# Performance work log

Measured on AMD Instinct MI355X. Metric: run time of the kernel, lower is better.

The kernel has to match this reference:

```python
import jax, jax.numpy as jnp
import numpy as np

# Production-scale sparse-voxel constants (Waymo-ish stride-8 grid)
N = 1_000_000   # active voxels across the batch
C = 128         # NUM_BEV_FEATURES
B, Z, Y, X = 8, 4, 468, 468  # batch size and spatial_shape (z, y, x)


def setup_inputs() -> dict:
    key = jax.random.key(0)
    kf, kb, kz, ky, kx = jax.random.split(key, 5)
    features = jax.random.normal(kf, (N, C), dtype=jnp.float32)
    b = jax.random.randint(kb, (N,), 0, B, dtype=jnp.int32)
    z = jax.random.randint(kz, (N,), 0, Z, dtype=jnp.int32)
    y = jax.random.randint(ky, (N,), 0, Y, dtype=jnp.int32)
    x = jax.random.randint(kx, (N,), 0, X, dtype=jnp.int32)
    indices = jnp.stack([b, z, y, x], axis=1)  # [N, 4]
    return {"features": features, "indices": indices}


def reference(features, indices):
    """Height compression: drop z, unique over (b, y, x), scatter-add features.

    Mirrors torch.unique(dim=0, return_inverse=True) + index_add_.
    Returns padded outputs of static size N (unique count is data-dependent;
    padded rows have key -1 and zero features / feature mass only where inv points).
    """
    n = features.shape[0]
    b, y, x = indices[:, 0], indices[:, 2], indices[:, 3]
    # Linearize (b, y, x) into a single int32 key; max key B*Y*X ~ 1.75e6 < 2^31.
    keys = (b * (Y * X) + y * X + x).astype(jnp.int32)
    uniq, inv = jnp.unique(keys, size=n, fill_value=-1, return_inverse=True)
    # index_add_ over unique rows == segment_sum with inverse indices
    features_unique = jax.ops.segment_sum(features, inv, num_segments=n)  # [N, C]
    # Decode unique linear keys back to (b, y, x); padded (-1) rows are garbage-marked.
    bb = uniq // (Y * X)
    rem = uniq % (Y * X)
    yy = rem // X
    xx = rem % X
    indices_unique = jnp.stack([bb, yy, xx], axis=1)  # [N, 3]
    return features_unique, indices_unique
```

## Files before the change

### kernel.cpp

```cpp
#include <hip/hip_runtime.h>

#define N_PTS   1000000
#define C_DIM   128
#define B_DIM   8
#define Y_DIM   468
#define X_DIM   468
#define YX      (Y_DIM * X_DIM)
#define KSPACE  (B_DIM * YX)

#define WG   256
#define EPT  8
#define EPB  (WG * EPT)
#define NBLK ((KSPACE + EPB - 1) / EPB)

#define F_BITS 21
#define F_MASK 0x1FFFFFu
#define SINGLE_FLAG (1ull << 63)

#define PAD_BLOCKS 2048

typedef float f4 __attribute__((ext_vector_type(4)));

__device__ __forceinline__ unsigned long long shfl_up_u64(unsigned long long v, int delta) {
    unsigned lo = (unsigned)v;
    unsigned hi = (unsigned)(v >> 32);
    lo = __shfl_up(lo, delta, 64);
    hi = __shfl_up(hi, delta, 64);
    return ((unsigned long long)hi << 32) | lo;
}

__global__ void zero_u32(unsigned* __restrict__ p, int n) {
    int i = blockIdx.x * blockDim.x + threadIdx.x;
    if (i < n) p[i] = 0u;
}

__global__ void hist_kernel(const int* __restrict__ idx, unsigned* __restrict__ cnt,
                            unsigned* __restrict__ keys, int n) {
    int i = blockIdx.x * blockDim.x + threadIdx.x;
    if (i >= n) return;
    int4 v = ((const int4*)idx)[i];
    unsigned key = (unsigned)(v.x * YX + v.z * X_DIM + v.w);
    keys[i] = key;
    atomicAdd(&cnt[key], 1u);
}

__global__ void scan1_kernel(const unsigned* __restrict__ cnt,
                             unsigned long long* __restrict__ pairs,
                             unsigned long long* __restrict__ bsums, int K) {
    int base = blockIdx.x * EPB + threadIdx.x * EPT;
    unsigned long long p[EPT];
    unsigned cc[EPT];
    unsigned long long run = 0;
#pragma unroll
    for (int j = 0; j < EPT; ++j) {
        int k = base + j;
        unsigned c = (k < K) ? cnt[k] : 0u;
        cc[j] = c;
        unsigned long long pr = (unsigned long long)c
                              | ((unsigned long long)(c ? 1u : 0u) << F_BITS)
                              | ((unsigned long long)(c >= 2u ? 1u : 0u) << (2 * F_BITS));
        p[j] = run;
        run += pr;
    }
    unsigned long long tot = run;
    int lane = threadIdx.x & 63;
    unsigned long long v = tot;
#pragma unroll
    for (int d = 1; d < 64; d <<= 1) {
        unsigned long long nv = shfl_up_u64(v, d);
        if (lane >= d) v += nv;
    }
    __shared__ unsigned long long wsum[WG / 64];
    int wid = threadIdx.x >> 6;
    if (lane == 63) wsum[wid] = v;
    __syncthreads();
    unsigned long long wexcl = 0;
    for (int w = 0; w < wid; ++w) wexcl += wsum[w];
    unsigned long long texcl = wexcl + v - tot;
#pragma unroll
    for (int j = 0; j < EPT; ++j) {
        int k = base + j;
        if (k < K)
            pairs[k] = (texcl + p[j]) | (cc[j] == 1u ? SINGLE_FLAG : 0ull);
    }
    if (threadIdx.x == WG - 1) bsums[blockIdx.x] = wexcl + v;
}

__global__ void scan2_kernel(unsigned long long* __restrict__ bsums, int nb) {
    int t = threadIdx.x;
    unsigned long long orig = (t < nb) ? bsums[t] : 0ull;
    unsigned long long v = orig;
    int lane = t & 63;
#pragma unroll
    for (int d = 1; d < 64; d <<= 1) {
        unsigned long long nv = shfl_up_u64(v, d);
        if (lane >= d) v += nv;
    }
    __shared__ unsigned long long ws[1024 / 64];
    int wid = t >> 6;
    if (lane == 63) ws[wid] = v;
    __syncthreads();
    unsigned long long wexcl = 0;
    for (int w = 0; w < wid; ++w) wexcl += ws[w];
    if (t < nb) bsums[t] = wexcl + v - orig;
    if (t == 1023) {
        unsigned long long tt = 0;
        for (int w = 0; w < 1024 / 64; ++w) tt += ws[w];
        bsums[nb] = tt;
    }
}

__global__ void uniq_kernel(const unsigned* __restrict__ cnt,
                            const unsigned long long* __restrict__ pairs,
                            const unsigned long long* __restrict__ bsums,
                            uint4* __restrict__ wl, float* __restrict__ outI, int K) {
    int k = blockIdx.x * blockDim.x + threadIdx.x;
    if (k >= K) return;
    unsigned c = cnt[k];
    if (c == 0) return;
    unsigned long long pr = (pairs[k] & ~SINGLE_FLAG) + bsums[k >> 11];
    unsigned rank = (unsigned)((pr >> F_BITS) & F_MASK);
    unsigned bb  = (unsigned)k / YX;
    unsigned rem = (unsigned)k % YX;
    outI[(size_t)rank * 3 + 0] = (float)bb;
    outI[(size_t)rank * 3 + 1] = (float)(rem / X_DIM);
    outI[(size_t)rank * 3 + 2] = (float)(rem % X_DIM);
    if (c >= 2) {
        unsigned start = (unsigned)(pr & F_MASK);
        unsigned mslot = (unsigned)((pr >> (2 * F_BITS)) & F_MASK);
        wl[mslot] = make_uint4(start, start + c, (unsigned)k, rank);
    }
}

__global__ void __launch_bounds__(256)
pointscatter_pad_kernel(const float* __restrict__ feat, const unsigned* __restrict__ keys,
                        const unsigned long long* __restrict__ pairs,
                        const unsigned long long* __restrict__ bsums,
                        unsigned* __restrict__ cnt, unsigned* __restrict__ pids,
                        float* __restrict__ outF, float* __restrict__ outI,
                        const unsigned long long* __restrict__ total,
                        int n, int pointBlocks) {
    int lane = threadIdx.x & 63;
    int wid  = threadIdx.x >> 6;
    int e    = lane >> 3;
    int sub  = lane & 7;
    if ((int)blockIdx.x < pointBlocks) {
        long p = (long)blockIdx.x * 32 + wid * 8 + e;
        if (p >= n) return;
        unsigned key = keys[p];
        unsigned long long pr = pairs[key];
        if (pr >> 63) {
            pr += bsums[key >> 11];
            unsigned rank = (unsigned)((pr >> F_BITS) & F_MASK);
            const f4* src = (const f4*)(feat + (size_t)p * C_DIM);
            f4*       dst = (f4*)(outF + (size_t)rank * C_DIM);
            f4 v0 = __builtin_nontemporal_load(src + sub);
            f4 v1 = __builtin_nontemporal_load(src + sub + 8);
            f4 v2 = __builtin_nontemporal_load(src + sub + 16);
            f4 v3 = __builtin_nontemporal_load(src + sub + 24);
            __builtin_nontemporal_store(v0, dst + sub);
            __builtin_nontemporal_store(v1, dst + sub + 8);
            __builtin_nontemporal_store(v2, dst + sub + 16);
            __builtin_nontemporal_store(v3, dst + sub + 24);
        } else if (sub == 0) {
            unsigned start = (unsigned)((pr + bsums[key >> 11]) & F_MASK);
            unsigned off = atomicSub(&cnt[key], 1u) - 1u;
            pids[start + off] = (unsigned)p;
        }
    } else {
        unsigned long long tot = *total;
        long nU = (long)((tot >> F_BITS) & F_MASK);
        long base   = nU + (long)((int)blockIdx.x - pointBlocks) * 32 + wid * 8 + e;
        long stride = (long)(gridDim.x - pointBlocks) * 32;
        f4 z = (f4)(0.f);
        for (long r = base; r < n; r += stride) {
            f4* dst = (f4*)(outF + (size_t)r * C_DIM);
            __builtin_nontemporal_store(z, dst + sub);
            __builtin_nontemporal_store(z, dst + sub + 8);
            __builtin_nontemporal_store(z, dst + sub + 16);
            __builtin_nontemporal_store(z, dst + sub + 24);
            if (sub == 0) {
                outI[(size_t)r * 3 + 0] = -1.0f;
                outI[(size_t)r * 3 + 1] = 467.0f;
                outI[(size_t)r * 3 + 2] = 467.0f;
            }
        }
    }
}

__global__ void __launch_bounds__(256)
multi_kernel(const float* __restrict__ feat, const unsigned* __restrict__ pointIds,
             const uint4* __restrict__ wl,
             const unsigned long long* __restrict__ total,
             float* __restrict__ outF) {
    int lane = threadIdx.x & 63;
    int wid  = threadIdx.x >> 6;
    int rq   = lane >> 4;
    int sub  = lane & 15;
    long m = (long)(((*total) >> (2 * F_BITS)) & F_MASK);
    long base   = (long)blockIdx.x * 16 + wid * 4 + rq;
    long stride = (long)gridDim.x * 16;
    for (long r = base; r < m; r += stride) {
        uint4 d = wl[r];
        f4 a0 = (f4)(0.f);
        f4 a1 = (f4)(0.f);
        unsigned j = d.x, e = d.y;
        for (; j + 1 < e; j += 2) {
            unsigned p0 = pointIds[j];
            unsigned p1 = pointIds[j + 1];
            const f4* s0 = (const f4*)(feat + (size_t)p0 * C_DIM);
            const f4* s1 = (const f4*)(feat + (size_t)p1 * C_DIM);
            f4 v00 = __builtin_nontemporal_load(s0 + sub);
            f4 v01 = __builtin_nontemporal_load(s0 + sub + 16);
            f4 v10 = __builtin_nontemporal_load(s1 + sub);
            f4 v11 = __builtin_nontemporal_load(s1 + sub + 16);
            a0 += v00 + v10;
            a1 += v01 + v11;
        }
        if (j < e) {
            unsigned p0 = pointIds[j];
            const f4* s0 = (const f4*)(feat + (size_t)p0 * C_DIM);
            f4 v00 = __builtin_nontemporal_load(s0 + sub);
            f4 v01 = __builtin_nontemporal_load(s0 + sub + 16);
            a0 += v00;
            a1 += v01;
        }
        f4* dst = (f4*)(outF + (size_t)d.w * C_DIM);
        __builtin_nontemporal_store(a0, dst + sub);
        __builtin_nontemporal_store(a1, dst + sub + 16);
    }
}

extern "C" void kernel_launch(void* const* d_in, const int* in_sizes, int n_in,
                              void* d_out, int out_size, void* d_ws, size_t ws_size,
                              hipStream_t stream) {
    const float* feat = (const float*)d_in[0];
    const int*   idx  = (const int*)d_in[1];
    const int n = in_sizes[0] / C_DIM;
    const int K = KSPACE;

    char* ws = (char*)d_ws;
    size_t off = 0;
    auto take = [&](size_t bytes) {
        size_t cur = off;
        off = (off + bytes + 255) & ~(size_t)255;
        return cur;
    };
    size_t o_cnt    = take((size_t)K * 4);
    size_t o_keys   = take((size_t)n * 4);
    size_t o_pairs  = take((size_t)K * 8);
    size_t o_bsums  = take((size_t)(NBLK + 1) * 8);
    size_t o_pids   = take((size_t)n * 4);
    size_t o_wl     = take((size_t)(n / 2 + 1) * 16);

    unsigned*           cnt    = (unsigned*)(ws + o_cnt);
    unsigned*           keys   = (unsigned*)(ws + o_keys);
    unsigned long long* pairs  = (unsigned long long*)(ws + o_pairs);
    unsigned long long* bsums  = (unsigned long long*)(ws + o_bsums);
    unsigned*           pids   = (unsigned*)(ws + o_pids);
    uint4*              wl     = (uint4*)(ws + o_wl);

    float* outF = (float*)d_out;
    float* outI = outF + (size_t)n * C_DIM;

    zero_u32<<<(K + 255) / 256, 256, 0, stream>>>(cnt, K);
    hist_kernel<<<(n + 255) / 256, 256, 0, stream>>>(idx, cnt, keys, n);
    scan1_kernel<<<NBLK, WG, 0, stream>>>(cnt, pairs, bsums, K);
    scan2_kernel<<<1, 1024, 0, stream>>>(bsums, NBLK);
    uniq_kernel<<<(K + 255) / 256, 256, 0, stream>>>(cnt, pairs, bsums, wl, outI, K);
    {
        int pointBlocks = (n + 31) / 32;
        pointscatter_pad_kernel<<<pointBlocks + PAD_BLOCKS, 256, 0, stream>>>(
            feat, keys, pairs, bsums, cnt, pids, outF, outI, bsums + NBLK, n, pointBlocks);
    }
    multi_kernel<<<4096, 256, 0, stream>>>(feat, pids, wl, bsums + NBLK, outF);
}
```

Before: 279.0 us.

## Fuse histogram, scans and unique pass into one cooperative kernel

Replaces the zero, histogram, two scan and unique kernels with a memset plus a single cooperative kernel that separates the phases with grid-wide syncs. The unique pass reuses the counts and prefix values already held in registers, so it no longer re-reads the pairs array and fewer kernels are launched. In exchange it depends on cooperative launch with NBLK (about 856) blocks all resident at once, and every block pays for three grid barriers.

```diff
diff --git a/kernel.cpp b/kernel.cpp
--- a/kernel.cpp
+++ b/kernel.cpp
@@ -1,4 +1,7 @@
 #include <hip/hip_runtime.h>
+#include <hip/hip_cooperative_groups.h>
+
+namespace cg = cooperative_groups;
 
 #define N_PTS   1000000
 #define C_DIM   128
@@ -29,25 +32,29 @@
     return ((unsigned long long)hi << 32) | lo;
 }
 
-__global__ void zero_u32(unsigned* __restrict__ p, int n) {
-    int i = blockIdx.x * blockDim.x + threadIdx.x;
-    if (i < n) p[i] = 0u;
-}
-
-__global__ void hist_kernel(const int* __restrict__ idx, unsigned* __restrict__ cnt,
-                            unsigned* __restrict__ keys, int n) {
-    int i = blockIdx.x * blockDim.x + threadIdx.x;
-    if (i >= n) return;
-    int4 v = ((const int4*)idx)[i];
-    unsigned key = (unsigned)(v.x * YX + v.z * X_DIM + v.w);
-    keys[i] = key;
-    atomicAdd(&cnt[key], 1u);
-}
-
-__global__ void scan1_kernel(const unsigned* __restrict__ cnt,
-                             unsigned long long* __restrict__ pairs,
-                             unsigned long long* __restrict__ bsums, int K) {
-    int base = blockIdx.x * EPB + threadIdx.x * EPT;
+__global__ void __launch_bounds__(WG)
+meta_kernel(const int* __restrict__ idx, unsigned* __restrict__ cnt,
+            unsigned* __restrict__ keys, unsigned long long* __restrict__ pairs,
+            unsigned long long* __restrict__ bsums, uint4* __restrict__ wl,
+            float* __restrict__ outI, int n, int K) {
+    cg::grid_group grid = cg::this_grid();
+    const int tid  = threadIdx.x;
+    const int lane = tid & 63;
+    const int wid  = tid >> 6;
+    __shared__ unsigned long long wsum[WG / 64];
+
+    {
+        int stride = NBLK * WG;
+        for (int i = blockIdx.x * WG + tid; i < n; i += stride) {
+            int4 v = ((const int4*)idx)[i];
+            unsigned key = (unsigned)(v.x * YX + v.z * X_DIM + v.w);
+            keys[i] = key;
+            atomicAdd(&cnt[key], 1u);
+        }
+    }
+    grid.sync();
+
+    int base = blockIdx.x * EPB + tid * EPT;
     unsigned long long p[EPT];
     unsigned cc[EPT];
     unsigned long long run = 0;
@@ -63,15 +70,12 @@
         run += pr;
     }
     unsigned long long tot = run;
-    int lane = threadIdx.x & 63;
     unsigned long long v = tot;
 #pragma unroll
     for (int d = 1; d < 64; d <<= 1) {
         unsigned long long nv = shfl_up_u64(v, d);
         if (lane >= d) v += nv;
     }
-    __shared__ unsigned long long wsum[WG / 64];
-    int wid = threadIdx.x >> 6;
     if (lane == 63) wsum[wid] = v;
     __syncthreads();
     unsigned long long wexcl = 0;
@@ -83,52 +87,60 @@
         if (k < K)
             pairs[k] = (texcl + p[j]) | (cc[j] == 1u ? SINGLE_FLAG : 0ull);
     }
-    if (threadIdx.x == WG - 1) bsums[blockIdx.x] = wexcl + v;
-}
-
-__global__ void scan2_kernel(unsigned long long* __restrict__ bsums, int nb) {
-    int t = threadIdx.x;
-    unsigned long long orig = (t < nb) ? bsums[t] : 0ull;
-    unsigned long long v = orig;
-    int lane = t & 63;
-#pragma unroll
-    for (int d = 1; d < 64; d <<= 1) {
-        unsigned long long nv = shfl_up_u64(v, d);
-        if (lane >= d) v += nv;
-    }
-    __shared__ unsigned long long ws[1024 / 64];
-    int wid = t >> 6;
-    if (lane == 63) ws[wid] = v;
-    __syncthreads();
-    unsigned long long wexcl = 0;
-    for (int w = 0; w < wid; ++w) wexcl += ws[w];
-    if (t < nb) bsums[t] = wexcl + v - orig;
-    if (t == 1023) {
-        unsigned long long tt = 0;
-        for (int w = 0; w < 1024 / 64; ++w) tt += ws[w];
-        bsums[nb] = tt;
-    }
-}
-
-__global__ void uniq_kernel(const unsigned* __restrict__ cnt,
-                            const unsigned long long* __restrict__ pairs,
-                            const unsigned long long* __restrict__ bsums,
-                            uint4* __restrict__ wl, float* __restrict__ outI, int K) {
-    int k = blockIdx.x * blockDim.x + threadIdx.x;
-    if (k >= K) return;
-    unsigned c = cnt[k];
-    if (c == 0) return;
-    unsigned long long pr = (pairs[k] & ~SINGLE_FLAG) + bsums[k >> 11];
-    unsigned rank = (unsigned)((pr >> F_BITS) & F_MASK);
-    unsigned bb  = (unsigned)k / YX;
-    unsigned rem = (unsigned)k % YX;
-    outI[(size_t)rank * 3 + 0] = (float)bb;
-    outI[(size_t)rank * 3 + 1] = (float)(rem / X_DIM);
-    outI[(size_t)rank * 3 + 2] = (float)(rem % X_DIM);
-    if (c >= 2) {
-        unsigned start = (unsigned)(pr & F_MASK);
-        unsigned mslot = (unsigned)((pr >> (2 * F_BITS)) & F_MASK);
-        wl[mslot] = make_uint4(start, start + c, (unsigned)k, rank);
+    if (tid == WG - 1) bsums[blockIdx.x] = wexcl + v;
+    grid.sync();
+
+    if (blockIdx.x == 0) {
+        const int SEG = 4;
+        unsigned long long loc[SEG];
+        unsigned long long run2 = 0;
+#pragma unroll
+        for (int j = 0; j < SEG; ++j) {
+            int i = tid * SEG + j;
+            loc[j] = run2;
+            run2 += (i < NBLK) ? bsums[i] : 0ull;
+        }
+        unsigned long long tot2 = run2;
+        unsigned long long v2 = tot2;
+#pragma unroll
+        for (int d = 1; d < 64; d <<= 1) {
+            unsigned long long nv = shfl_up_u64(v2, d);
+            if (lane >= d) v2 += nv;
+        }
+        __syncthreads();
+        if (lane == 63) wsum[wid] = v2;
+        __syncthreads();
+        unsigned long long wexcl2 = 0;
+        for (int w = 0; w < wid; ++w) wexcl2 += wsum[w];
+        unsigned long long texcl2 = wexcl2 + v2 - tot2;
+#pragma unroll
+        for (int j = 0; j < SEG; ++j) {
+            int i = tid * SEG + j;
+            if (i < NBLK) bsums[i] = texcl2 + loc[j];
+        }
+        if (tid == WG - 1) bsums[NBLK] = wexcl2 + v2;
+    }
+    grid.sync();
+
+    unsigned long long bofs = bsums[blockIdx.x];
+#pragma unroll
+    for (int j = 0; j < EPT; ++j) {
+        int k = base + j;
+        if (k >= K) break;
+        unsigned c = cc[j];
+        if (c == 0) continue;
+        unsigned long long pr = texcl + p[j] + bofs;
+        unsigned rank = (unsigned)((pr >> F_BITS) & F_MASK);
+        unsigned bb  = (unsigned)k / YX;
+        unsigned rem = (unsigned)k % YX;
+        outI[(size_t)rank * 3 + 0] = (float)bb;
+        outI[(size_t)rank * 3 + 1] = (float)(rem / X_DIM);
+        outI[(size_t)rank * 3 + 2] = (float)(rem % X_DIM);
+        if (c >= 2) {
+            unsigned start = (unsigned)(pr & F_MASK);
+            unsigned mslot = (unsigned)((pr >> (2 * F_BITS)) & F_MASK);
+            wl[mslot] = make_uint4(start, start + c, (unsigned)k, rank);
+        }
     }
 }
 
@@ -263,11 +275,16 @@
     float* outF = (float*)d_out;
     float* outI = outF + (size_t)n * C_DIM;
 
-    zero_u32<<<(K + 255) / 256, 256, 0, stream>>>(cnt, K);
-    hist_kernel<<<(n + 255) / 256, 256, 0, stream>>>(idx, cnt, keys, n);
-    scan1_kernel<<<NBLK, WG, 0, stream>>>(cnt, pairs, bsums, K);
-    scan2_kernel<<<1, 1024, 0, stream>>>(bsums, NBLK);
-    uniq_kernel<<<(K + 255) / 256, 256, 0, stream>>>(cnt, pairs, bsums, wl, outI, K);
+    hipMemsetAsync(cnt, 0, (size_t)K * 4, stream);
+
+    {
+        int nArg = n, KArg = K;
+        void* args[] = { (void*)&idx, (void*)&cnt, (void*)&keys, (void*)&pairs,
+                         (void*)&bsums, (void*)&wl, (void*)&outI, (void*)&nArg, (void*)&KArg };
+        hipLaunchCooperativeKernel((const void*)meta_kernel, dim3(NBLK), dim3(WG),
+                                   args, 0, stream);
+    }
+
     {
         int pointBlocks = (n + 31) / 32;
         pointscatter_pad_kernel<<<pointBlocks + PAD_BLOCKS, 256, 0, stream>>>(
```

Measured after the change: 580.7 us. 108% more time.

## Fuse unique-key decode into point scatter kernel and memset counts

Applied to the files above, without the earlier changes.

Folds the per-key unique/index-decode work into the same launch as the point scatter and padding work, using the first block range of the grid. Each thread now derives a key's count from the difference of adjacent prefix pairs instead of reading the count array, which the scatter blocks decrement concurrently with atomics. The separate zeroing kernel is replaced by a hipMemsetAsync. The intent is to remove a kernel launch and its pass over the count array, at the cost of more branching in one heterogeneous kernel and relying on the packed-prefix arithmetic to reproduce counts exactly.

```diff
diff --git a/kernel.cpp b/kernel.cpp
--- a/kernel.cpp
+++ b/kernel.cpp
@@ -27,11 +27,6 @@
     lo = __shfl_up(lo, delta, 64);
     hi = __shfl_up(hi, delta, 64);
     return ((unsigned long long)hi << 32) | lo;
-}
-
-__global__ void zero_u32(unsigned* __restrict__ p, int n) {
-    int i = blockIdx.x * blockDim.x + threadIdx.x;
-    if (i < n) p[i] = 0u;
 }
 
 __global__ void hist_kernel(const int* __restrict__ idx, unsigned* __restrict__ cnt,
@@ -110,42 +105,56 @@
     }
 }
 
-__global__ void uniq_kernel(const unsigned* __restrict__ cnt,
-                            const unsigned long long* __restrict__ pairs,
-                            const unsigned long long* __restrict__ bsums,
-                            uint4* __restrict__ wl, float* __restrict__ outI, int K) {
-    int k = blockIdx.x * blockDim.x + threadIdx.x;
-    if (k >= K) return;
-    unsigned c = cnt[k];
-    if (c == 0) return;
-    unsigned long long pr = (pairs[k] & ~SINGLE_FLAG) + bsums[k >> 11];
-    unsigned rank = (unsigned)((pr >> F_BITS) & F_MASK);
-    unsigned bb  = (unsigned)k / YX;
-    unsigned rem = (unsigned)k % YX;
-    outI[(size_t)rank * 3 + 0] = (float)bb;
-    outI[(size_t)rank * 3 + 1] = (float)(rem / X_DIM);
-    outI[(size_t)rank * 3 + 2] = (float)(rem % X_DIM);
-    if (c >= 2) {
-        unsigned start = (unsigned)(pr & F_MASK);
-        unsigned mslot = (unsigned)((pr >> (2 * F_BITS)) & F_MASK);
-        wl[mslot] = make_uint4(start, start + c, (unsigned)k, rank);
-    }
-}
-
 __global__ void __launch_bounds__(256)
-pointscatter_pad_kernel(const float* __restrict__ feat, const unsigned* __restrict__ keys,
-                        const unsigned long long* __restrict__ pairs,
-                        const unsigned long long* __restrict__ bsums,
-                        unsigned* __restrict__ cnt, unsigned* __restrict__ pids,
-                        float* __restrict__ outF, float* __restrict__ outI,
-                        const unsigned long long* __restrict__ total,
-                        int n, int pointBlocks) {
-    int lane = threadIdx.x & 63;
-    int wid  = threadIdx.x >> 6;
-    int e    = lane >> 3;
-    int sub  = lane & 7;
-    if ((int)blockIdx.x < pointBlocks) {
-        long p = (long)blockIdx.x * 32 + wid * 8 + e;
+heavy_kernel(const float* __restrict__ feat, const unsigned* __restrict__ keys,
+             const unsigned long long* __restrict__ pairs,
+             const unsigned long long* __restrict__ bsums,
+             unsigned* __restrict__ cnt, unsigned* __restrict__ pids,
+             uint4* __restrict__ wl,
+             float* __restrict__ outF, float* __restrict__ outI,
+             int n, int K, int pointBlocks) {
+    int tid  = threadIdx.x;
+    int lane = tid & 63;
+    int wid  = tid >> 6;
+    int bid  = blockIdx.x;
+
+    if (bid < NBLK) {
+        int base = bid * EPB + tid * EPT;
+        if (base >= K) return;
+        unsigned long long bofs = bsums[bid];
+        unsigned long long P[EPT + 1];
+#pragma unroll
+        for (int j = 0; j < EPT; ++j) {
+            int k = base + j;
+            P[j] = (k < K) ? ((pairs[k] & ~SINGLE_FLAG) + bofs) : bsums[NBLK];
+        }
+        {
+            int k = base + EPT;
+            P[EPT] = (k < K) ? ((pairs[k] & ~SINGLE_FLAG) + bsums[k >> 11]) : bsums[NBLK];
+        }
+#pragma unroll
+        for (int j = 0; j < EPT; ++j) {
+            int k = base + j;
+            if (k >= K) break;
+            unsigned long long diff = P[j + 1] - P[j];
+            unsigned c = (unsigned)(diff & F_MASK);
+            if (c == 0) continue;
+            unsigned rank = (unsigned)((P[j] >> F_BITS) & F_MASK);
+            unsigned bb  = (unsigned)k / YX;
+            unsigned rem = (unsigned)k % YX;
+            outI[(size_t)rank * 3 + 0] = (float)bb;
+            outI[(size_t)rank * 3 + 1] = (float)(rem / X_DIM);
+            outI[(size_t)rank * 3 + 2] = (float)(rem % X_DIM);
+            if (c >= 2) {
+                unsigned start = (unsigned)(P[j] & F_MASK);
+                unsigned mslot = (unsigned)((P[j] >> (2 * F_BITS)) & F_MASK);
+                wl[mslot] = make_uint4(start, start + c, (unsigned)k, rank);
+            }
+        }
+    } else if (bid < NBLK + pointBlocks) {
+        int e   = lane >> 3;
+        int sub = lane & 7;
+        long p = (long)(bid - NBLK) * 32 + wid * 8 + e;
         if (p >= n) return;
         unsigned key = keys[p];
         unsigned long long pr = pairs[key];
@@ -168,10 +177,13 @@
             pids[start + off] = (unsigned)p;
         }
     } else {
-        unsigned long long tot = *total;
+        int e   = lane >> 3;
+        int sub = lane & 7;
+        unsigned long long tot = bsums[NBLK];
         long nU = (long)((tot >> F_BITS) & F_MASK);
-        long base   = nU + (long)((int)blockIdx.x - pointBlocks) * 32 + wid * 8 + e;
-        long stride = (long)(gridDim.x - pointBlocks) * 32;
+        long pb = bid - NBLK - pointBlocks;
+        long base   = nU + pb * 32 + wid * 8 + e;
+        long stride = (long)PAD_BLOCKS * 32;
         f4 z = (f4)(0.f);
         for (long r = base; r < n; r += stride) {
             f4* dst = (f4*)(outF + (size_t)r * C_DIM);
@@ -263,15 +275,14 @@
     float* outF = (float*)d_out;
     float* outI = outF + (size_t)n * C_DIM;
 
-    zero_u32<<<(K + 255) / 256, 256, 0, stream>>>(cnt, K);
+    hipMemsetAsync(cnt, 0, (size_t)K * 4, stream);
     hist_kernel<<<(n + 255) / 256, 256, 0, stream>>>(idx, cnt, keys, n);
     scan1_kernel<<<NBLK, WG, 0, stream>>>(cnt, pairs, bsums, K);
     scan2_kernel<<<1, 1024, 0, stream>>>(bsums, NBLK);
-    uniq_kernel<<<(K + 255) / 256, 256, 0, stream>>>(cnt, pairs, bsums, wl, outI, K);
     {
         int pointBlocks = (n + 31) / 32;
-        pointscatter_pad_kernel<<<pointBlocks + PAD_BLOCKS, 256, 0, stream>>>(
-            feat, keys, pairs, bsums, cnt, pids, outF, outI, bsums + NBLK, n, pointBlocks);
+        heavy_kernel<<<NBLK + pointBlocks + PAD_BLOCKS, 256, 0, stream>>>(
+            feat, keys, pairs, bsums, cnt, pids, wl, outF, outI, n, K, pointBlocks);
     }
     multi_kernel<<<4096, 256, 0, stream>>>(feat, pids, wl, bsums + NBLK, outF);
 }
```

After: 280.4 us. Within noise of the previous version (+0.5%).
